# Kernel optimization log

Hardware: AMD Instinct MI355X
Metric: run time of the kernel (lower is better)

The kernel has to match this reference:

```python
import jax, jax.numpy as jnp
import numpy as np

B_SZ, SEQ_LEN, STATE_DIM, D_IN, D_OUT, KX = 8, 2048, 1024, 512, 512, 10


def setup_inputs() -> dict:
    key = jax.random.key(0)
    ks = jax.random.split(key, 7)
    inputs = jax.random.normal(ks[0], (B_SZ, SEQ_LEN, D_IN), dtype=jnp.float32)
    h0 = jax.random.normal(ks[1], (STATE_DIM,), dtype=jnp.float32)
    # exponential_decay_init(lam=15): x = clamp(-1/lam * log(1-u), max=1); A = (1-x)*sign
    u = jax.random.uniform(ks[2], (STATE_DIM,), dtype=jnp.float32)
    x = jnp.minimum(-(1.0 / 15.0) * jnp.log1p(-u), 1.0)
    sign = jnp.sign(jax.random.normal(ks[3], (STATE_DIM,), dtype=jnp.float32))
    A = (1.0 - x) * sign
    Bm = jax.random.normal(ks[4], (D_IN, STATE_DIM), dtype=jnp.float32) / D_IN
    C = jax.random.normal(ks[5], (STATE_DIM, D_OUT), dtype=jnp.float32) / STATE_DIM
    M = jax.random.normal(ks[6], (D_OUT, D_IN, KX), dtype=jnp.float32) / D_OUT
    return {"inputs": inputs, "h0": h0, "A": A, "B": Bm, "C": C, "M": M}


def _ar_preds(M, x):
    # Equivalent to einsum('oik,bli->bklo') + per-k roll + triu mask + sum over k:
    # ar[b,l,:] = sum_{i=0}^{k-1, i<=l} M[:,:,i] @ x[b, l-i, :]
    b, l, d_in = x.shape
    kx = M.shape[2]
    ar = jnp.einsum('oi,bli->blo', M[:, :, 0], x)
    for i in range(1, kx):
        x_shift = jnp.pad(x, ((0, 0), (i, 0), (0, 0)))[:, :l]  # shift right, zero-fill
        ar = ar + jnp.einsum('oi,bli->blo', M[:, :, i], x_shift)
    return ar


def reference(inputs, h0, A, B, C, M):
    b, l, d_in = inputs.shape
    state_dim = A.shape[0]
    # Project inputs once: u_t @ B for all t -> [b, l, s]
    uB = jnp.einsum('bli,is->bls', inputs, B)

    def step(h, u_t):
        h = A * h + u_t  # diagonal recurrence
        return h, h

    h_init = jnp.broadcast_to(h0, (b, state_dim))
    _, hs = jax.lax.scan(step, h_init, jnp.swapaxes(uB, 0, 1))  # [l, b, s]
    hs = jnp.swapaxes(hs, 0, 1)  # [b, l, s]
    lds_out = hs @ C  # [b, l, d_out]
    return lds_out + _ar_preds(M, inputs)
```

## Files before the change

kernel.cpp:

```cpp
#include <hip/hip_runtime.h>

#define B_SZ   8
#define SEQ    2048
#define PSEQ   (SEQ+16)
#define SDIM   1024
#define DIN    512
#define DOUT   512
#define KX     10
#define RTOT   (B_SZ*SEQ)
#define LC     64
#define NC     (SEQ/LC)

typedef __attribute__((ext_vector_type(8))) short short8;
typedef __attribute__((ext_vector_type(4))) float f32x4;
typedef __attribute__((ext_vector_type(4))) unsigned short bfx4;

#define OFF_XP   0UL
#define OFF_UB   16973824UL
#define OFF_HS   50528256UL
#define OFF_BT   84082688UL
#define OFF_CT   85131264UL
#define OFF_MT   86179840UL

__device__ __forceinline__ short f2bf(float f) {
  unsigned u = __builtin_bit_cast(unsigned, f);
  u += 0x7fffu + ((u >> 16) & 1u);
  return (short)(u >> 16);
}
__device__ __forceinline__ float bf2f(unsigned short b) {
  return __builtin_bit_cast(float, (unsigned)b << 16);
}

#define GLOAD16(gp, lp) __builtin_amdgcn_global_load_lds( \
    (const __attribute__((address_space(1))) void*)(gp), \
    (__attribute__((address_space(3))) void*)(lp), 16, 0, 0)
#define WAITVM(n) asm volatile("s_waitcnt vmcnt(" #n ")" ::: "memory")
#define LGKM0()   do { asm volatile("s_waitcnt lgkmcnt(0)" ::: "memory"); \
                       __builtin_amdgcn_sched_barrier(0); } while (0)
#define SBAR() __builtin_amdgcn_s_barrier()

__global__ void k_prep1(const float* __restrict__ x, const float* __restrict__ B,
                        short* __restrict__ Xp, short* __restrict__ Bt) {
  __shared__ float t[32][33];
  int blk = blockIdx.x, tid = threadIdx.x;
  if (blk < 2048) {
    const int NG = RTOT * (DIN / 8);
    const int NPAD = B_SZ * 16 * (DIN / 8);
    for (int g = blk * 256 + tid; g < NG + NPAD; g += 2048 * 256) {
      if (g < NG) {
        int r = g >> 6, c8 = g & 63;
        int b = r >> 11, tt = r & 2047;
        const float4* p = reinterpret_cast<const float4*>(x) + (size_t)g * 2;
        float4 f0 = p[0], f1 = p[1];
        short8 o;
        o[0]=f2bf(f0.x); o[1]=f2bf(f0.y); o[2]=f2bf(f0.z); o[3]=f2bf(f0.w);
        o[4]=f2bf(f1.x); o[5]=f2bf(f1.y); o[6]=f2bf(f1.z); o[7]=f2bf(f1.w);
        *reinterpret_cast<short8*>(Xp + ((size_t)(b * PSEQ + 16 + tt) * DIN + c8 * 8)) = o;
      } else {
        int idx = g - NG;
        int b = idx >> 10, rem = idx & 1023;
        int row16 = rem >> 6, c8 = rem & 63;
        const short8 z = {0,0,0,0,0,0,0,0};
        *reinterpret_cast<short8*>(Xp + ((size_t)(b * PSEQ + row16) * DIN + c8 * 8)) = z;
      }
    }
  } else {
    int idx = blk - 2048;
    int bx = (idx & 31) * 32, by = (idx >> 5) * 32;
    int tx = tid & 31, ty = tid >> 5;
    #pragma unroll
    for (int j = 0; j < 32; j += 8)
      t[ty + j][tx] = B[(size_t)(by + ty + j) * SDIM + (bx + tx)];
    __syncthreads();
    #pragma unroll
    for (int j = 0; j < 32; j += 8)
      Bt[(size_t)(bx + ty + j) * DIN + (by + tx)] = f2bf(t[tx][ty + j]);
  }
}

__global__ void k_scan_h(const short* __restrict__ uB, const float* __restrict__ A,
                         const float* __restrict__ h0, const float* __restrict__ E,
                         short* __restrict__ hs,
                         const float* __restrict__ C, const float* __restrict__ M,
                         short* __restrict__ Ct, short* __restrict__ Mt) {
  __shared__ float t[32][33];
  int blk = blockIdx.x, tid = threadIdx.x;
  if (blk < 256) {
    int b = blk >> 5, c = blk & 31;
    int s0 = tid * 4;
    float a[4], h[4], ap[4];
    #pragma unroll
    for (int j = 0; j < 4; ++j) {
      a[j] = A[s0 + j];
      float p = a[j];
      #pragma unroll
      for (int q = 0; q < 6; ++q) p *= p;
      ap[j] = p;
      h[j] = h0[s0 + j];
    }
    const float* Eb = E + (size_t)b * NC * SDIM + s0;
    for (int c2 = 0; c2 < c; ++c2) {
      float4 ev = *reinterpret_cast<const float4*>(Eb + (size_t)c2 * SDIM);
      h[0] = fmaf(ap[0], h[0], ev.x);
      h[1] = fmaf(ap[1], h[1], ev.y);
      h[2] = fmaf(ap[2], h[2], ev.z);
      h[3] = fmaf(ap[3], h[3], ev.w);
    }
    const short* base = uB + ((size_t)b * SEQ + (size_t)c * LC) * SDIM + s0;
    short* hbase = hs + ((size_t)b * SEQ + (size_t)c * LC) * SDIM + s0;
    for (int tt = 0; tt < LC; ++tt) {
      bfx4 v = *reinterpret_cast<const bfx4*>(base + (size_t)tt * SDIM);
      bfx4 o;
      #pragma unroll
      for (int j = 0; j < 4; ++j) {
        h[j] = fmaf(a[j], h[j], bf2f(v[j]));
        o[j] = (unsigned short)f2bf(h[j]);
      }
      *reinterpret_cast<bfx4*>(hbase + (size_t)tt * SDIM) = o;
    }
  } else if (blk < 768) {
    int idx = blk - 256;
    int bx = (idx & 15) * 32, by = (idx >> 4) * 32;
    int tx = tid & 31, ty = tid >> 5;
    #pragma unroll
    for (int j = 0; j < 32; j += 8)
      t[ty + j][tx] = C[(size_t)(by + ty + j) * DOUT + (bx + tx)];
    __syncthreads();
    #pragma unroll
    for (int j = 0; j < 32; j += 8)
      Ct[(size_t)(bx + ty + j) * SDIM + (by + tx)] = f2bf(t[tx][ty + j]);
  } else {
    int idx = (blk - 768) * 256 + tid;
    if (idx < DOUT * DIN) {
      int o = idx / DIN, i = idx - o * DIN;
      const float* src = M + ((size_t)o * DIN + i) * KX;
      #pragma unroll
      for (int tt = 0; tt < KX; ++tt)
        Mt[((size_t)tt * DOUT + o) * DIN + i] = f2bf(src[tt]);
    }
  }
}

__device__ __forceinline__ void stage128(const short* __restrict__ g, int ld,
                                         short* l, int tid) {
  int rsub = tid >> 3;
  int slot = (tid & 7) ^ (rsub & 7);
  #pragma unroll
  for (int i = 0; i < 4; ++i) {
    int row = i * 32 + rsub;
    GLOAD16(g + (size_t)row * ld + slot * 8, l + row * 64 + (tid & 7) * 8);
  }
}

__device__ __forceinline__ void mfma_tile(const short* lA, int aoff, const short* lB,
                                          int lane, int wm, int wn, f32x4 acc[4][4]) {
  int lr = lane & 15;
  int h  = lane >> 4;
  #pragma unroll
  for (int kk = 0; kk < 2; ++kk) {
    int kslot = kk * 4 + h;
    short8 af[4], bfr[4];
    #pragma unroll
    for (int mi = 0; mi < 4; ++mi) {
      int row = aoff + wm * 64 + mi * 16 + lr;
      af[mi] = *reinterpret_cast<const short8*>(lA + row * 64 + ((kslot ^ (row & 7)) << 3));
    }
    #pragma unroll
    for (int ni = 0; ni < 4; ++ni) {
      int row = wn * 64 + ni * 16 + lr;
      bfr[ni] = *reinterpret_cast<const short8*>(lB + row * 64 + ((kslot ^ (row & 7)) << 3));
    }
    __builtin_amdgcn_s_setprio(1);
    #pragma unroll
    for (int mi = 0; mi < 4; ++mi)
      #pragma unroll
      for (int ni = 0; ni < 4; ++ni)
        acc[mi][ni] = __builtin_amdgcn_mfma_f32_16x16x32_bf16(af[mi], bfr[ni], acc[mi][ni], 0, 0, 0);
    __builtin_amdgcn_s_setprio(0);
  }
}

__global__ __launch_bounds__(256) void k_gemm_uB(const short* __restrict__ Xp,
                                                 const short* __restrict__ Bt,
                                                 short* __restrict__ uB,
                                                 const float* __restrict__ Adecay,
                                                 float* __restrict__ E) {
  __shared__ __attribute__((aligned(16))) short lds[32768];
  short* A0 = lds;         short* B0 = lds + 8192;
  short* A1 = lds + 16384; short* B1 = lds + 24576;
  int tid = threadIdx.x, lane = tid & 63, w = tid >> 6, wm = w >> 1, wn = w & 1;
  long r0 = (long)blockIdx.x * 128;
  int  c0 = blockIdx.y * 128;
  int  b  = (int)(r0 >> 11);
  const short* Abase = Xp + (size_t)(r0 + 16 * (b + 1)) * DIN;
  const short* Bbase = Bt + (size_t)c0 * DIN;
  const f32x4 z4 = {0.f, 0.f, 0.f, 0.f};
  f32x4 acc[4][4];
  #pragma unroll
  for (int mi = 0; mi < 4; ++mi)
    #pragma unroll
    for (int ni = 0; ni < 4; ++ni) acc[mi][ni] = z4;

  stage128(Abase, DIN, A0, tid);      stage128(Bbase, DIN, B0, tid);
  stage128(Abase + 64, DIN, A1, tid); stage128(Bbase + 64, DIN, B1, tid);
  WAITVM(8);
  SBAR();
  for (int kt = 0; kt < 8; ++kt) {
    const short* a  = (kt & 1) ? A1 : A0;
    const short* bb = (kt & 1) ? B1 : B0;
    mfma_tile(a, 0, bb, lane, wm, wn, acc);
    SBAR();
    if (kt + 2 < 8) {
      short* ad = (kt & 1) ? A1 : A0;
      short* bd = (kt & 1) ? B1 : B0;
      stage128(Abase + (kt + 2) * 64, DIN, ad, tid);
      stage128(Bbase + (kt + 2) * 64, DIN, bd, tid);
      WAITVM(8);
    } else {
      WAITVM(0);
    }
    SBAR();
  }
  int h = lane >> 4;
  #pragma unroll
  for (int mi = 0; mi < 4; ++mi)
    #pragma unroll
    for (int ni = 0; ni < 4; ++ni)
      #pragma unroll
      for (int r = 0; r < 4; ++r) {
        long row = r0 + wm * 64 + mi * 16 + h * 4 + r;
        int  col = c0 + wn * 64 + ni * 16 + (lane & 15);
        uB[(size_t)row * SDIM + col] = f2bf(acc[mi][ni][r]);
      }
  int cch = (int)((r0 >> 6) & 31) + wm;
  #pragma unroll
  for (int ni = 0; ni < 4; ++ni) {
    int col = c0 + wn * 64 + ni * 16 + (lane & 15);
    float a  = Adecay[col];
    float a2 = a * a, a3 = a2 * a;
    float A4 = a2 * a2;
    float A16 = A4 * A4; A16 = A16 * A16;
    float P16_2 = A16 * A16, P16_3 = P16_2 * A16;
    float Q4 = (h == 3) ? 1.f : (h == 2) ? A4 : (h == 1) ? A4 * A4 : A4 * A4 * A4;
    float cm0 = fmaf(acc[0][ni][0], a3, fmaf(acc[0][ni][1], a2, fmaf(acc[0][ni][2], a, acc[0][ni][3])));
    float cm1 = fmaf(acc[1][ni][0], a3, fmaf(acc[1][ni][1], a2, fmaf(acc[1][ni][2], a, acc[1][ni][3])));
    float cm2 = fmaf(acc[2][ni][0], a3, fmaf(acc[2][ni][1], a2, fmaf(acc[2][ni][2], a, acc[2][ni][3])));
    float cm3 = fmaf(acc[3][ni][0], a3, fmaf(acc[3][ni][1], a2, fmaf(acc[3][ni][2], a, acc[3][ni][3])));
    float L = fmaf(cm0, P16_3, fmaf(cm1, P16_2, fmaf(cm2, A16, cm3)));
    L *= Q4;
    L += __shfl_xor(L, 16);
    L += __shfl_xor(L, 32);
    if (h == 0) E[((size_t)b * NC + cch) * SDIM + col] = L;
  }
}

struct Frags { short8 a[4][2]; short8 b[4][2]; };

__device__ __forceinline__ void read_frags(Frags& f, const short* la, int aoff,
                                           const short* lb, int lane, int wm, int wn) {
  int lr = lane & 15, h = lane >> 4;
  #pragma unroll
  for (int kk = 0; kk < 2; ++kk) {
    int kslot = kk * 4 + h;
    #pragma unroll
    for (int mi = 0; mi < 4; ++mi) {
      int row = aoff + wm * 64 + mi * 16 + lr;
      f.a[mi][kk] = *reinterpret_cast<const short8*>(la + row * 64 + ((kslot ^ (row & 7)) << 3));
    }
    #pragma unroll
    for (int ni = 0; ni < 4; ++ni) {
      int row = wn * 64 + ni * 16 + lr;
      f.b[ni][kk] = *reinterpret_cast<const short8*>(lb + row * 64 + ((kslot ^ (row & 7)) << 3));
    }
  }
}

__device__ __forceinline__ void mfma_frags(const Frags& f, f32x4 acc[4][4]) {
  #pragma unroll
  for (int kk = 0; kk < 2; ++kk)
    #pragma unroll
    for (int mi = 0; mi < 4; ++mi)
      #pragma unroll
      for (int ni = 0; ni < 4; ++ni)
        acc[mi][ni] = __builtin_amdgcn_mfma_f32_16x16x32_bf16(f.a[mi][kk], f.b[ni][kk], acc[mi][ni], 0, 0, 0);
}

__device__ __forceinline__ void sgb_interleave() {
  #pragma unroll
  for (int i = 0; i < 16; ++i) {
    __builtin_amdgcn_sched_group_barrier(0x008, 2, 0);
    __builtin_amdgcn_sched_group_barrier(0x100, 1, 0);
  }
}

__device__ __forceinline__ void stageA256(const short* __restrict__ g, int ld,
                                          short* l, int tid) {
  int rsub = tid >> 3;
  int slot = (tid & 7) ^ (rsub & 7);
  #pragma unroll
  for (int i = 0; i < 4; ++i) {
    int row = i * 64 + rsub;
    GLOAD16(g + (size_t)row * ld + slot * 8, l + row * 64 + (tid & 7) * 8);
  }
}
__device__ __forceinline__ void stageB128(const short* __restrict__ g, int ld,
                                          short* l, int tid) {
  int rsub = tid >> 3;
  int slot = (tid & 7) ^ (rsub & 7);
  #pragma unroll
  for (int i = 0; i < 2; ++i) {
    int row = i * 64 + rsub;
    GLOAD16(g + (size_t)row * ld + slot * 8, l + row * 64 + (tid & 7) * 8);
  }
}
__device__ __forceinline__ void stageX320(const short* __restrict__ g,
                                          short* l, int tid) {
  int rsub = tid >> 3;
  int slot = (tid & 7) ^ (rsub & 7);
  #pragma unroll
  for (int i = 0; i < 5; ++i) {
    int row = i * 64 + rsub;
    GLOAD16(g + (size_t)row * DIN + slot * 8, l + row * 64 + (tid & 7) * 8);
  }
}

__global__ __launch_bounds__(512, 2) void k_gemm_out(const short* __restrict__ hs,
                                                     const short* __restrict__ Xp,
                                                     const short* __restrict__ Ct,
                                                     const short* __restrict__ Mt,
                                                     float* __restrict__ out) {
  __shared__ __attribute__((aligned(16))) short lds[81920];
  short* const P0  = lds;
  short* const P1  = lds + 24576;
  short* const P2  = lds + 49152;
  short* const Xs0 = lds;
  short* const Xs1 = lds + 20480;
  short* const PM0 = lds + 57344;
  short* const PM1 = lds + 65536;
  short* const PM2 = lds + 73728;
  int tid = threadIdx.x, lane = tid & 63, w = tid >> 6;
  int wm = w >> 1, wn = w & 1;
  int bid = blockIdx.x;
  int sw  = (bid & 7) * 32 + (bid >> 3);
  long r0 = (long)(sw & 63) * 256;
  int  c0 = (sw >> 6) * 128;
  int  b  = (int)(r0 >> 11);
  const short* hsA = hs + (size_t)r0 * SDIM;
  const short* CtB = Ct + (size_t)c0 * SDIM;
  const short* Xa  = Xp + (size_t)(r0 + 16 * (b + 1) - 16) * DIN;
  const short* MtB = Mt + (size_t)c0 * DIN;

  const f32x4 z4 = {0.f, 0.f, 0.f, 0.f};
  f32x4 acc[4][4];
  #pragma unroll
  for (int mi = 0; mi < 4; ++mi)
    #pragma unroll
    for (int ni = 0; ni < 4; ++ni) acc[mi][ni] = z4;

  Frags fr[2];

  stageA256(hsA,        SDIM, P0, tid);  stageB128(CtB,        SDIM, P0 + 16384, tid);
  stageA256(hsA + 64,   SDIM, P1, tid);  stageB128(CtB + 64,   SDIM, P1 + 16384, tid);
  stageA256(hsA + 128,  SDIM, P2, tid);  stageB128(CtB + 128,  SDIM, P2 + 16384, tid);
  WAITVM(6);
  SBAR();
  read_frags(fr[0], P0, 0, P0 + 16384, lane, wm, wn);

  #pragma unroll
  for (int s = 0; s < 16; ++s) {
    __builtin_amdgcn_s_setprio(1);
    mfma_frags(fr[s & 1], acc);
    if (s < 15) {
      const short* nb = ((s + 1) % 3 == 0) ? P0 : ((s + 1) % 3 == 1) ? P1 : P2;
      read_frags(fr[(s + 1) & 1], nb, 0, nb + 16384, lane, wm, wn);
    } else {
      read_frags(fr[0], Xs0, 16, PM0, lane, wm, wn);
    }
    sgb_interleave();
    __builtin_amdgcn_s_setprio(0);
    LGKM0();
    SBAR();
    if (s <= 12) {
      short* sp = (s % 3 == 0) ? P0 : (s % 3 == 1) ? P1 : P2;
      stageA256(hsA + (s + 3) * 64, SDIM, sp, tid);
      stageB128(CtB + (s + 3) * 64, SDIM, sp + 16384, tid);
      WAITVM(6);
    } else if (s == 13) {
      stageB128(MtB, DIN, PM0, tid);
      stageB128(MtB + (size_t)DOUT * DIN, DIN, PM1, tid);
      WAITVM(4);
    } else if (s == 14) {
      stageB128(MtB + (size_t)2 * DOUT * DIN, DIN, PM2, tid);
      stageX320(Xa, Xs0, tid);
      WAITVM(0);
    }
    SBAR();
  }

  for (int k0 = 0; k0 < 8; ++k0) {
    int kc = k0 * 64;
    const short* xs = (k0 & 1) ? Xs1 : Xs0;
    short*       xn = (k0 & 1) ? Xs0 : Xs1;
    const short* q0 = (k0 % 3 == 0) ? PM0 : (k0 % 3 == 1) ? PM1 : PM2;
    const short* q1 = (k0 % 3 == 0) ? PM1 : (k0 % 3 == 1) ? PM2 : PM0;
    const short* q2 = (k0 % 3 == 0) ? PM2 : (k0 % 3 == 1) ? PM0 : PM1;
    #pragma unroll
    for (int j = 0; j < KX; ++j) {
      __builtin_amdgcn_s_setprio(1);
      mfma_frags(fr[j & 1], acc);
      bool do_read = (j < 9) || (k0 < 7);
      if (j < 9) {
        const short* mn = ((j + 1) % 3 == 0) ? q0 : ((j + 1) % 3 == 1) ? q1 : q2;
        read_frags(fr[(j + 1) & 1], xs, 15 - j, mn, lane, wm, wn);
      } else if (k0 < 7) {
        read_frags(fr[0], xn, 16, q1, lane, wm, wn);
      }
      if (do_read) sgb_interleave();
      __builtin_amdgcn_s_setprio(0);
      LGKM0();
      SBAR();
      if (j + 3 <= 9) {
        short* mw = (j % 3 == 0) ? (short*)q0 : (j % 3 == 1) ? (short*)q1 : (short*)q2;
        stageB128(MtB + (size_t)(j + 3) * DOUT * DIN + kc, DIN, mw, tid);
      } else if (k0 < 7) {
        short* mw = (j % 3 == 0) ? (short*)q0 : (j % 3 == 1) ? (short*)q1 : (short*)q2;
        stageB128(MtB + (size_t)(j - 7) * DOUT * DIN + kc + 64, DIN, mw, tid);
      }
      if (j == 1 && k0 < 7) stageX320(Xa + kc + 64, xn, tid);
      if (j == 1 || j == 2) {
        if (k0 < 7) { WAITVM(7); } else { WAITVM(2); }
      } else if (j >= 7) {
        if (k0 == 7) { WAITVM(0); } else { WAITVM(2); }
      } else {
        WAITVM(2);
      }
      SBAR();
    }
  }

  #pragma unroll
  for (int mi = 0; mi < 4; ++mi)
    #pragma unroll
    for (int ni = 0; ni < 4; ++ni)
      #pragma unroll
      for (int r = 0; r < 4; ++r) {
        long row = r0 + wm * 64 + mi * 16 + (lane >> 4) * 4 + r;
        int  col = c0 + wn * 64 + ni * 16 + (lane & 15);
        out[(size_t)row * DOUT + col] = acc[mi][ni][r];
      }
}

extern "C" void kernel_launch(void* const* d_in, const int* in_sizes, int n_in,
                              void* d_out, int out_size, void* d_ws, size_t ws_size,
                              hipStream_t stream) {
  (void)in_sizes; (void)n_in; (void)out_size; (void)ws_size;
  const float* x  = (const float*)d_in[0];
  const float* h0 = (const float*)d_in[1];
  const float* A  = (const float*)d_in[2];
  const float* B  = (const float*)d_in[3];
  const float* C  = (const float*)d_in[4];
  const float* M  = (const float*)d_in[5];
  float* out = (float*)d_out;
  char* ws = (char*)d_ws;

  short* Xp  = (short*)(ws + OFF_XP);
  short* uB  = (short*)(ws + OFF_UB);
  short* hsb = (short*)(ws + OFF_HS);
  short* Bt  = (short*)(ws + OFF_BT);
  short* Ct  = (short*)(ws + OFF_CT);
  short* Mt  = (short*)(ws + OFF_MT);
  float* E   = out;

  k_prep1<<<2560, 256, 0, stream>>>(x, B, Xp, Bt);
  k_gemm_uB<<<dim3(RTOT / 128, SDIM / 128), 256, 0, stream>>>(Xp, Bt, uB, A, E);
  k_scan_h<<<1792, 256, 0, stream>>>(uB, A, h0, E, hsb, C, M, Ct, Mt);
  k_gemm_out<<<256, 512, 0, stream>>>(hsb, Xp, Ct, Mt, out);
}
```

Before: 147.0 us.

## Restructure uB GEMM with 256-row tiles, triple-buffered LDS and register prefetch

The input-projection GEMM now uses 512-thread blocks covering 256x128 output tiles, with three LDS stages and double-buffered register fragments. MFMA issue is interleaved with the next stage's LDS fragment reads through sched_group_barrier, the same pipeline already used in the output GEMM. The goal is to hide LDS and global-load latency and cut barrier stalls per k-step. In exchange it uses more LDS (about 144KB per block) and more registers, which limits occupancy to two blocks and leaves only 512 blocks in the grid.

New measurement: 146.9 us (median of 2 runs). Within noise of the previous version (-0.1%).

```diff
diff --git a/kernel.cpp b/kernel.cpp
--- a/kernel.cpp
+++ b/kernel.cpp
@@ -38,6 +38,76 @@
 #define LGKM0()   do { asm volatile("s_waitcnt lgkmcnt(0)" ::: "memory"); \
                        __builtin_amdgcn_sched_barrier(0); } while (0)
 #define SBAR() __builtin_amdgcn_s_barrier()
+
+struct Frags { short8 a[4][2]; short8 b[4][2]; };
+
+__device__ __forceinline__ void read_frags(Frags& f, const short* la, int aoff,
+                                           const short* lb, int lane, int wm, int wn) {
+  int lr = lane & 15, h = lane >> 4;
+  #pragma unroll
+  for (int kk = 0; kk < 2; ++kk) {
+    int kslot = kk * 4 + h;
+    #pragma unroll
+    for (int mi = 0; mi < 4; ++mi) {
+      int row = aoff + wm * 64 + mi * 16 + lr;
+      f.a[mi][kk] = *reinterpret_cast<const short8*>(la + row * 64 + ((kslot ^ (row & 7)) << 3));
+    }
+    #pragma unroll
+    for (int ni = 0; ni < 4; ++ni) {
+      int row = wn * 64 + ni * 16 + lr;
+      f.b[ni][kk] = *reinterpret_cast<const short8*>(lb + row * 64 + ((kslot ^ (row & 7)) << 3));
+    }
+  }
+}
+
+__device__ __forceinline__ void mfma_frags(const Frags& f, f32x4 acc[4][4]) {
+  #pragma unroll
+  for (int kk = 0; kk < 2; ++kk)
+    #pragma unroll
+    for (int mi = 0; mi < 4; ++mi)
+      #pragma unroll
+      for (int ni = 0; ni < 4; ++ni)
+        acc[mi][ni] = __builtin_amdgcn_mfma_f32_16x16x32_bf16(f.a[mi][kk], f.b[ni][kk], acc[mi][ni], 0, 0, 0);
+}
+
+__device__ __forceinline__ void sgb_interleave() {
+  #pragma unroll
+  for (int i = 0; i < 16; ++i) {
+    __builtin_amdgcn_sched_group_barrier(0x008, 2, 0);
+    __builtin_amdgcn_sched_group_barrier(0x100, 1, 0);
+  }
+}
+
+__device__ __forceinline__ void stageA256(const short* __restrict__ g, int ld,
+                                          short* l, int tid) {
+  int rsub = tid >> 3;
+  int slot = (tid & 7) ^ (rsub & 7);
+  #pragma unroll
+  for (int i = 0; i < 4; ++i) {
+    int row = i * 64 + rsub;
+    GLOAD16(g + (size_t)row * ld + slot * 8, l + row * 64 + (tid & 7) * 8);
+  }
+}
+__device__ __forceinline__ void stageB128(const short* __restrict__ g, int ld,
+                                          short* l, int tid) {
+  int rsub = tid >> 3;
+  int slot = (tid & 7) ^ (rsub & 7);
+  #pragma unroll
+  for (int i = 0; i < 2; ++i) {
+    int row = i * 64 + rsub;
+    GLOAD16(g + (size_t)row * ld + slot * 8, l + row * 64 + (tid & 7) * 8);
+  }
+}
+__device__ __forceinline__ void stageX320(const short* __restrict__ g,
+                                          short* l, int tid) {
+  int rsub = tid >> 3;
+  int slot = (tid & 7) ^ (rsub & 7);
+  #pragma unroll
+  for (int i = 0; i < 5; ++i) {
+    int row = i * 64 + rsub;
+    GLOAD16(g + (size_t)row * DIN + slot * 8, l + row * 64 + (tid & 7) * 8);
+  }
+}
 
 __global__ void k_prep1(const float* __restrict__ x, const float* __restrict__ B,
                         short* __restrict__ Xp, short* __restrict__ Bt) {
@@ -141,59 +211,24 @@
   }
 }
 
-__device__ __forceinline__ void stage128(const short* __restrict__ g, int ld,
-                                         short* l, int tid) {
-  int rsub = tid >> 3;
-  int slot = (tid & 7) ^ (rsub & 7);
-  #pragma unroll
-  for (int i = 0; i < 4; ++i) {
-    int row = i * 32 + rsub;
-    GLOAD16(g + (size_t)row * ld + slot * 8, l + row * 64 + (tid & 7) * 8);
-  }
-}
-
-__device__ __forceinline__ void mfma_tile(const short* lA, int aoff, const short* lB,
-                                          int lane, int wm, int wn, f32x4 acc[4][4]) {
-  int lr = lane & 15;
-  int h  = lane >> 4;
-  #pragma unroll
-  for (int kk = 0; kk < 2; ++kk) {
-    int kslot = kk * 4 + h;
-    short8 af[4], bfr[4];
-    #pragma unroll
-    for (int mi = 0; mi < 4; ++mi) {
-      int row = aoff + wm * 64 + mi * 16 + lr;
-      af[mi] = *reinterpret_cast<const short8*>(lA + row * 64 + ((kslot ^ (row & 7)) << 3));
-    }
-    #pragma unroll
-    for (int ni = 0; ni < 4; ++ni) {
-      int row = wn * 64 + ni * 16 + lr;
-      bfr[ni] = *reinterpret_cast<const short8*>(lB + row * 64 + ((kslot ^ (row & 7)) << 3));
-    }
-    __builtin_amdgcn_s_setprio(1);
-    #pragma unroll
-    for (int mi = 0; mi < 4; ++mi)
-      #pragma unroll
-      for (int ni = 0; ni < 4; ++ni)
-        acc[mi][ni] = __builtin_amdgcn_mfma_f32_16x16x32_bf16(af[mi], bfr[ni], acc[mi][ni], 0, 0, 0);
-    __builtin_amdgcn_s_setprio(0);
-  }
-}
-
-__global__ __launch_bounds__(256) void k_gemm_uB(const short* __restrict__ Xp,
-                                                 const short* __restrict__ Bt,
-                                                 short* __restrict__ uB,
-                                                 const float* __restrict__ Adecay,
-                                                 float* __restrict__ E) {
-  __shared__ __attribute__((aligned(16))) short lds[32768];
-  short* A0 = lds;         short* B0 = lds + 8192;
-  short* A1 = lds + 16384; short* B1 = lds + 24576;
-  int tid = threadIdx.x, lane = tid & 63, w = tid >> 6, wm = w >> 1, wn = w & 1;
-  long r0 = (long)blockIdx.x * 128;
-  int  c0 = blockIdx.y * 128;
+__global__ __launch_bounds__(512, 2) void k_gemm_uB(const short* __restrict__ Xp,
+                                                    const short* __restrict__ Bt,
+                                                    short* __restrict__ uB,
+                                                    const float* __restrict__ Adecay,
+                                                    float* __restrict__ E) {
+  __shared__ __attribute__((aligned(16))) short lds[73728];
+  short* const P0 = lds;
+  short* const P1 = lds + 24576;
+  short* const P2 = lds + 49152;
+  int tid = threadIdx.x, lane = tid & 63, w = tid >> 6;
+  int wm = w >> 1, wn = w & 1;
+  int bid = blockIdx.x;
+  long r0 = (long)(bid & 63) * 256;
+  int  c0 = (bid >> 6) * 128;
   int  b  = (int)(r0 >> 11);
-  const short* Abase = Xp + (size_t)(r0 + 16 * (b + 1)) * DIN;
-  const short* Bbase = Bt + (size_t)c0 * DIN;
+  const short* Aa = Xp + (size_t)(r0 + 16 * (b + 1)) * DIN;
+  const short* Bb = Bt + (size_t)c0 * DIN;
+
   const f32x4 z4 = {0.f, 0.f, 0.f, 0.f};
   f32x4 acc[4][4];
   #pragma unroll
@@ -201,26 +236,40 @@
     #pragma unroll
     for (int ni = 0; ni < 4; ++ni) acc[mi][ni] = z4;
 
-  stage128(Abase, DIN, A0, tid);      stage128(Bbase, DIN, B0, tid);
-  stage128(Abase + 64, DIN, A1, tid); stage128(Bbase + 64, DIN, B1, tid);
-  WAITVM(8);
+  Frags fr[2];
+
+  stageA256(Aa,       DIN, P0, tid);  stageB128(Bb,       DIN, P0 + 16384, tid);
+  stageA256(Aa + 64,  DIN, P1, tid);  stageB128(Bb + 64,  DIN, P1 + 16384, tid);
+  stageA256(Aa + 128, DIN, P2, tid);  stageB128(Bb + 128, DIN, P2 + 16384, tid);
+  WAITVM(6);
   SBAR();
-  for (int kt = 0; kt < 8; ++kt) {
-    const short* a  = (kt & 1) ? A1 : A0;
-    const short* bb = (kt & 1) ? B1 : B0;
-    mfma_tile(a, 0, bb, lane, wm, wn, acc);
-    SBAR();
-    if (kt + 2 < 8) {
-      short* ad = (kt & 1) ? A1 : A0;
-      short* bd = (kt & 1) ? B1 : B0;
-      stage128(Abase + (kt + 2) * 64, DIN, ad, tid);
-      stage128(Bbase + (kt + 2) * 64, DIN, bd, tid);
-      WAITVM(8);
-    } else {
-      WAITVM(0);
-    }
-    SBAR();
-  }
+  read_frags(fr[0], P0, 0, P0 + 16384, lane, wm, wn);
+
+  #pragma unroll
+  for (int s = 0; s < 8; ++s) {
+    __builtin_amdgcn_s_setprio(1);
+    mfma_frags(fr[s & 1], acc);
+    if (s < 7) {
+      const short* nb = ((s + 1) % 3 == 0) ? P0 : ((s + 1) % 3 == 1) ? P1 : P2;
+      read_frags(fr[(s + 1) & 1], nb, 0, nb + 16384, lane, wm, wn);
+      sgb_interleave();
+    }
+    __builtin_amdgcn_s_setprio(0);
+    if (s < 7) {
+      LGKM0();
+      SBAR();
+      if (s <= 4) {
+        short* sp = (s % 3 == 0) ? P0 : (s % 3 == 1) ? P1 : P2;
+        stageA256(Aa + (s + 3) * 64, DIN, sp, tid);
+        stageB128(Bb + (s + 3) * 64, DIN, sp + 16384, tid);
+        WAITVM(6);
+      } else {
+        WAITVM(0);
+      }
+      SBAR();
+    }
+  }
+
   int h = lane >> 4;
   #pragma unroll
   for (int mi = 0; mi < 4; ++mi)
@@ -251,76 +300,6 @@
     L += __shfl_xor(L, 16);
     L += __shfl_xor(L, 32);
     if (h == 0) E[((size_t)b * NC + cch) * SDIM + col] = L;
-  }
-}
-
-struct Frags { short8 a[4][2]; short8 b[4][2]; };
-
-__device__ __forceinline__ void read_frags(Frags& f, const short* la, int aoff,
-                                           const short* lb, int lane, int wm, int wn) {
-  int lr = lane & 15, h = lane >> 4;
-  #pragma unroll
-  for (int kk = 0; kk < 2; ++kk) {
-    int kslot = kk * 4 + h;
-    #pragma unroll
-    for (int mi = 0; mi < 4; ++mi) {
-      int row = aoff + wm * 64 + mi * 16 + lr;
-      f.a[mi][kk] = *reinterpret_cast<const short8*>(la + row * 64 + ((kslot ^ (row & 7)) << 3));
-    }
-    #pragma unroll
-    for (int ni = 0; ni < 4; ++ni) {
-      int row = wn * 64 + ni * 16 + lr;
-      f.b[ni][kk] = *reinterpret_cast<const short8*>(lb + row * 64 + ((kslot ^ (row & 7)) << 3));
-    }
-  }
-}
-
-__device__ __forceinline__ void mfma_frags(const Frags& f, f32x4 acc[4][4]) {
-  #pragma unroll
-  for (int kk = 0; kk < 2; ++kk)
-    #pragma unroll
-    for (int mi = 0; mi < 4; ++mi)
-      #pragma unroll
-      for (int ni = 0; ni < 4; ++ni)
-        acc[mi][ni] = __builtin_amdgcn_mfma_f32_16x16x32_bf16(f.a[mi][kk], f.b[ni][kk], acc[mi][ni], 0, 0, 0);
-}
-
-__device__ __forceinline__ void sgb_interleave() {
-  #pragma unroll
-  for (int i = 0; i < 16; ++i) {
-    __builtin_amdgcn_sched_group_barrier(0x008, 2, 0);
-    __builtin_amdgcn_sched_group_barrier(0x100, 1, 0);
-  }
-}
-
-__device__ __forceinline__ void stageA256(const short* __restrict__ g, int ld,
-                                          short* l, int tid) {
-  int rsub = tid >> 3;
-  int slot = (tid & 7) ^ (rsub & 7);
-  #pragma unroll
-  for (int i = 0; i < 4; ++i) {
-    int row = i * 64 + rsub;
-    GLOAD16(g + (size_t)row * ld + slot * 8, l + row * 64 + (tid & 7) * 8);
-  }
-}
-__device__ __forceinline__ void stageB128(const short* __restrict__ g, int ld,
-                                          short* l, int tid) {
-  int rsub = tid >> 3;
-  int slot = (tid & 7) ^ (rsub & 7);
-  #pragma unroll
-  for (int i = 0; i < 2; ++i) {
-    int row = i * 64 + rsub;
-    GLOAD16(g + (size_t)row * ld + slot * 8, l + row * 64 + (tid & 7) * 8);
-  }
-}
-__device__ __forceinline__ void stageX320(const short* __restrict__ g,
-                                          short* l, int tid) {
-  int rsub = tid >> 3;
-  int slot = (tid & 7) ^ (rsub & 7);
-  #pragma unroll
-  for (int i = 0; i < 5; ++i) {
-    int row = i * 64 + rsub;
-    GLOAD16(g + (size_t)row * DIN + slot * 8, l + row * 64 + (tid & 7) * 8);
   }
 }
 
@@ -472,7 +451,7 @@
   float* E   = out;
 
   k_prep1<<<2560, 256, 0, stream>>>(x, B, Xp, Bt);
-  k_gemm_uB<<<dim3(RTOT / 128, SDIM / 128), 256, 0, stream>>>(Xp, Bt, uB, A, E);
+  k_gemm_uB<<<512, 512, 0, stream>>>(Xp, Bt, uB, A, E);
   k_scan_h<<<1792, 256, 0, stream>>>(uB, A, h0, E, hsb, C, M, Ct, Mt);
   k_gemm_out<<<256, 512, 0, stream>>>(hsb, Xp, Ct, Mt, out);
 }
```
